# Performance work log

Hardware: AMD Instinct MI355X
Metric: run time of the kernel (lower is better)

Reference implementation:

```python
import jax, jax.numpy as jnp
import numpy as np

THRESHOLD = 1.0
BETA = 0.9  # initial mem is zeros, so mem = beta*0 + u = u


def spike(u):
    # forward of SurrogateGradient: (u > threshold).float()
    return (u > THRESHOLD).astype(u.dtype)


def rope_tables(seq_len, head_dim, base=10000.0):
    inv_freq = 1.0 / (base ** (jnp.arange(0, head_dim, 2, dtype=jnp.float32) / head_dim))
    t = jnp.arange(seq_len, dtype=jnp.float32)
    freqs = jnp.einsum('i,j->ij', t, inv_freq)          # [S, d/2]
    emb = jnp.concatenate([freqs, freqs], axis=-1)       # [S, d]
    return jnp.cos(emb), jnp.sin(emb)


def apply_rope(x, cos, sin):
    # x: [B, S, H, d]
    x1, x2 = jnp.split(x, 2, axis=-1)
    rot = jnp.concatenate([-x2, x1], axis=-1)
    return x * cos[None, :, None, :] + rot * sin[None, :, None, :]


def setup_inputs() -> dict:
    key = jax.random.key(0)
    ks = jax.random.split(key, 5)
    B, S, D = 1, 2048, 2048
    std = 1.0 / np.sqrt(D)
    return {
        'x':  jax.random.normal(ks[0], (B, S, D), jnp.float32),
        'Wq': jax.random.normal(ks[1], (D, D), jnp.float32) * std,
        'Wk': jax.random.normal(ks[2], (D, D), jnp.float32) * std,
        'Wv': jax.random.normal(ks[3], (D, D), jnp.float32) * std,
        'Wo': jax.random.normal(ks[4], (D, D), jnp.float32) * std,
    }


def reference(x, Wq, Wk, Wv, Wo):
    B, S, D = x.shape
    H, hd = 16, 128
    scale = hd ** -0.5

    q = (x @ Wq).reshape(B, S, H, hd)
    k = (x @ Wk).reshape(B, S, H, hd)
    v = (x @ Wv).reshape(B, S, H, hd)

    # LIF: mem starts at zero -> mem = q; spike = (mem > threshold)
    sq, sk, sv = spike(q), spike(k), spike(v)

    cos, sin = rope_tables(S, hd)
    rq = apply_rope(sq, cos, sin)
    rk = apply_rope(sk, cos, sin)

    scores = jnp.einsum('bqhd,bkhd->bhqk', rq, rk) * scale  # [B,H,S,S]
    causal = jnp.tril(jnp.ones((S, S), dtype=bool))
    scores = jnp.where(causal[None, None], scores, -jnp.inf)
    attn = jax.nn.softmax(scores, axis=-1)

    out = jnp.einsum('bhqk,bkhd->bqhd', attn, sv).reshape(B, S, H * hd)
    return out @ Wo
```

## Files before the change

kernel.cpp:

```cpp
#include <hip/hip_runtime.h>

typedef unsigned short u16;
typedef unsigned int u32;
typedef u16 u16x4 __attribute__((ext_vector_type(4)));
typedef u16 u16x8 __attribute__((ext_vector_type(8)));
typedef float f32x4 __attribute__((ext_vector_type(4)));
typedef __bf16 bf16x8 __attribute__((ext_vector_type(8)));
typedef _Float16 f16x4 __attribute__((ext_vector_type(4)));
typedef _Float16 f16x8 __attribute__((ext_vector_type(8)));

#define DD 2048
#define SCALE_ATTN 0.08838834764831845f
#define DELTA 0.005f

#define GL16(g, l)                                                              \
  __builtin_amdgcn_global_load_lds((const __attribute__((address_space(1))) u32*)(g), \
                                   (__attribute__((address_space(3))) u32*)(l), 16, 0, 0)

__device__ __forceinline__ u16 f2bf(float f) {
  u32 u = __float_as_uint(f);
  u32 r = (u + 0x7FFFu + ((u >> 16) & 1u)) >> 16;
  return (u16)r;
}
__device__ __forceinline__ float bf2f(u16 h) { return __uint_as_float(((u32)h) << 16); }


__global__ void k_rope_tables(float* __restrict__ cosT, float* __restrict__ sinT) {
  int i = blockIdx.x * 256 + threadIdx.x;
  int s = i >> 6, j = i & 63;
  float e = (float)(2 * j) / 128.0f;
  float inv = 1.0f / powf(10000.0f, e);
  float fr = (float)s * inv;
  cosT[i] = cosf(fr);
  sinT[i] = sinf(fr);
}

__global__ void k_cvt_x(const float* __restrict__ x, _Float16* __restrict__ xf) {
  int i = (blockIdx.x * 256 + threadIdx.x) * 4;
  float4 v = *(const float4*)&x[i];
  f16x4 o = {(_Float16)v.x, (_Float16)v.y, (_Float16)v.z, (_Float16)v.w};
  *(f16x4*)&xf[i] = o;
}

__global__ void k_transpose_w(const float* __restrict__ Wq, const float* __restrict__ Wk,
                              const float* __restrict__ Wv, _Float16* __restrict__ Wq16,
                              _Float16* __restrict__ Wk16, _Float16* __restrict__ Wv16,
                              float* __restrict__ Wq32, float* __restrict__ Wk32,
                              float* __restrict__ Wv32) {
  const float* W = blockIdx.y == 0 ? Wq : (blockIdx.y == 1 ? Wk : Wv);
  _Float16* WT16 = blockIdx.y == 0 ? Wq16 : (blockIdx.y == 1 ? Wk16 : Wv16);
  float* WT32 = blockIdx.y == 0 ? Wq32 : (blockIdx.y == 1 ? Wk32 : Wv32);
  __shared__ float tile[32][33];
  int bk = blockIdx.x & 63, bn = blockIdx.x >> 6;
  int c = threadIdx.x & 31, r0 = threadIdx.x >> 5;
#pragma unroll
  for (int i = 0; i < 4; ++i) {
    int r = r0 + i * 8;
    tile[r][c] = W[(size_t)(bk * 32 + r) * DD + bn * 32 + c];
  }
  __syncthreads();
#pragma unroll
  for (int i = 0; i < 4; ++i) {
    int r = r0 + i * 8;
    float v = tile[c][r];
    size_t o = (size_t)(bn * 32 + r) * DD + bk * 32 + c;
    WT16[o] = (_Float16)v;
    WT32[o] = v;
  }
}

__global__ void k_transpose_bo(const float* __restrict__ W, u16* __restrict__ WhT) {
  __shared__ float tile[32][33];
  int bk = blockIdx.x & 63, bn = blockIdx.x >> 6;
  int c = threadIdx.x & 31, r0 = threadIdx.x >> 5;
#pragma unroll
  for (int i = 0; i < 4; ++i) {
    int r = r0 + i * 8;
    tile[r][c] = W[(size_t)(bk * 32 + r) * DD + bn * 32 + c];
  }
  __syncthreads();
#pragma unroll
  for (int i = 0; i < 4; ++i) {
    int r = r0 + i * 8;
    WhT[(size_t)(bn * 32 + r) * DD + bk * 32 + c] = f2bf(tile[c][r]);
  }
}

__global__ void k_transpose_bf16(const u16* __restrict__ in, u16* __restrict__ out) {
  __shared__ u16 tile[32][33];
  int bk = blockIdx.x & 63, bn = blockIdx.x >> 6;
  int c = threadIdx.x & 31, r0 = threadIdx.x >> 5;
#pragma unroll
  for (int i = 0; i < 4; ++i) {
    int r = r0 + i * 8;
    tile[r][c] = in[(size_t)(bk * 32 + r) * DD + bn * 32 + c];
  }
  __syncthreads();
#pragma unroll
  for (int i = 0; i < 4; ++i) {
    int r = r0 + i * 8;
    out[(size_t)(bn * 32 + r) * DD + bk * 32 + c] = tile[c][r];
  }
}

__global__ void k_rope_apply(u16* sq, u16* sk, const float* __restrict__ cosT,
                             const float* __restrict__ sinT) {
  int i = blockIdx.x * 256 + threadIdx.x;
  int s = i >> 10;
  int rest = i & 1023;
  int h = rest >> 6, j = rest & 63;
  size_t base = (size_t)s * DD + h * 128 + j;
  float c = cosT[(s << 6) | j], sn = sinT[(s << 6) | j];
  float a = bf2f(sq[base]), b = bf2f(sq[base + 64]);
  sq[base] = f2bf(a * c - b * sn);
  sq[base + 64] = f2bf(b * c + a * sn);
  a = bf2f(sk[base]);
  b = bf2f(sk[base + 64]);
  sk[base] = f2bf(a * c - b * sn);
  sk[base + 64] = f2bf(b * c + a * sn);
}

__global__ __launch_bounds__(256) void k_gemm_qkv(
    const _Float16* __restrict__ xf, const _Float16* __restrict__ BqT,
    const _Float16* __restrict__ BkT, const _Float16* __restrict__ BvT, u16* __restrict__ Sq,
    u16* __restrict__ Sk, u16* __restrict__ Sv, unsigned char* __restrict__ flagT) {
  __shared__ u16 lA[2 * 4096];
  __shared__ u16 lB[2 * 4096];

  const _Float16* BT = blockIdx.y == 0 ? BqT : (blockIdx.y == 1 ? BkT : BvT);
  u16* Out = blockIdx.y == 0 ? Sq : (blockIdx.y == 1 ? Sk : Sv);
  unsigned char* flT = flagT + (size_t)blockIdx.y * 4194304;

  int bid = blockIdx.x;
  int swz = (bid & 7) * 32 + (bid >> 3);
  int m0 = (swz >> 4) * 128, n0 = (swz & 15) * 128;

  int tid = threadIdx.x;
  int lane = tid & 63;
  int w = tid >> 6;
  int wr = (w >> 1) * 64, wc = (w & 1) * 64;
  int l15 = lane & 15, g8 = (lane >> 4) * 8;

  int ar0 = tid >> 2, ac0 = (tid & 3) << 3;
  int ar1 = (tid + 256) >> 2, ac1 = (tid & 3) << 3;

  f32x4 zero = {0.f, 0.f, 0.f, 0.f};
  f32x4 acc[4][4];
#pragma unroll
  for (int i = 0; i < 4; ++i)
#pragma unroll
    for (int j = 0; j < 4; ++j) acc[i][j] = zero;

  u16* laBase0 = lA + w * 512;
  u16* laBase1 = lA + 2048 + w * 512;
  u16* lbBase0 = lB + w * 512;
  u16* lbBase1 = lB + 2048 + w * 512;

  auto stage = [&](int buf, int vs) {
    int k0 = vs << 5;
    int bo = buf * 4096;
    GL16(&xf[(size_t)(m0 + ar0) * DD + k0 + ac0], laBase0 + bo);
    GL16(&xf[(size_t)(m0 + ar1) * DD + k0 + ac1], laBase1 + bo);
    GL16(&BT[(size_t)(n0 + ar0) * DD + k0 + ac0], lbBase0 + bo);
    GL16(&BT[(size_t)(n0 + ar1) * DD + k0 + ac1], lbBase1 + bo);
  };

  stage(0, 0);
  __syncthreads();
  for (int vs = 0; vs < 64; ++vs) {
    int cur = vs & 1;
    if (vs + 1 < 64) stage(cur ^ 1, vs + 1);
    const u16* la = lA + cur * 4096;
    const u16* lb = lB + cur * 4096;
    f16x8 af[4], bfr[4];
#pragma unroll
    for (int i = 0; i < 4; ++i) af[i] = *(const f16x8*)&la[(wr + i * 16 + l15) * 32 + g8];
#pragma unroll
    for (int j = 0; j < 4; ++j) bfr[j] = *(const f16x8*)&lb[(wc + j * 16 + l15) * 32 + g8];
#pragma unroll
    for (int i = 0; i < 4; ++i)
#pragma unroll
      for (int j = 0; j < 4; ++j)
        acc[i][j] = __builtin_amdgcn_mfma_f32_16x16x32_f16(af[i], bfr[j], acc[i][j], 0, 0, 0);
    __syncthreads();
  }

  int g4 = (lane >> 4) * 4;
#pragma unroll
  for (int i = 0; i < 4; ++i) {
    int row0 = m0 + wr + i * 16 + g4;
#pragma unroll
    for (int j = 0; j < 4; ++j) {
      int col = n0 + wc + j * 16 + l15;
      u32 fw = 0;
#pragma unroll
      for (int r = 0; r < 4; ++r) {
        float u = acc[i][j][r];
        Out[(size_t)(row0 + r) * DD + col] = (u > 1.0f) ? (u16)0x3F80 : (u16)0;
        if (fabsf(u - 1.0f) < DELTA) fw |= (1u << (8 * r));
      }
      *(u32*)&flT[(size_t)col * 2048 + row0] = fw;
    }
  }
}

__global__ __launch_bounds__(256) void k_compact(const unsigned char* __restrict__ flagT,
                                                 u32* __restrict__ cnt, u32* __restrict__ wlist) {
  __shared__ u32 wsum[4];
  int tid = threadIdx.x;
  int lane = tid & 63;
  int w = tid >> 6;
  size_t blockBase = (size_t)blockIdx.x * 16384;
  const u32* fp = (const u32*)(flagT + blockBase);
  unsigned long long fm = 0;
#pragma unroll
  for (int it = 0; it < 4; ++it) {
    u32 m16 = 0;
#pragma unroll
    for (int wd = 0; wd < 4; ++wd) {
      u32 v = fp[it * 1024 + tid * 4 + wd];
      m16 |= (((v >> 0) & 1u) | ((v >> 7) & 2u) | ((v >> 14) & 4u) | ((v >> 21) & 8u)) << (wd * 4);
    }
    fm |= (unsigned long long)m16 << (it * 16);
  }
  u32 c = (u32)__popcll(fm);
  u32 pre = c;
#pragma unroll
  for (int d = 1; d < 64; d <<= 1) {
    u32 t = __shfl_up(pre, d, 64);
    if (lane >= d) pre += t;
  }
  if (lane == 63) wsum[w] = pre;
  __syncthreads();
  u32 wbase = 0;
#pragma unroll
  for (int i = 0; i < 4; ++i)
    if (i < w) wbase += wsum[i];
  if (tid == 0) {
    u32 tot = wsum[0] + wsum[1] + wsum[2] + wsum[3];
    cnt[blockIdx.x] = tot > 256u ? 256u : tot;
  }
  u32 pos = wbase + pre - c;
  u32 outbase = (u32)blockIdx.x * 256u;
  while (fm) {
    int p = __ffsll((long long)fm) - 1;
    fm &= fm - 1;
    u32 e = (u32)blockBase + (u32)(p >> 4) * 4096u + (u32)tid * 16u + (u32)(p & 15);
    if (pos < 256u) wlist[outbase + pos] = e;
    ++pos;
  }
}

__global__ __launch_bounds__(256) void k_fixup(
    const float* __restrict__ x, const float* __restrict__ WqT, const float* __restrict__ WkT,
    const float* __restrict__ WvT, const u32* __restrict__ cnt, const u32* __restrict__ wlist,
    u16* __restrict__ Sq, u16* __restrict__ Sk, u16* __restrict__ Sv) {
  u32 wid = (blockIdx.x * 256 + threadIdx.x) >> 6;
  int lane = threadIdx.x & 63;
  for (u32 s = wid; s < 768u * 256u; s += 8192u) {
    u32 b = s % 768u, k = s / 768u;
    if (k >= cnt[b]) continue;
    u32 e = wlist[b * 256u + k];
    int i = (int)(e & 2047u);
    int j = (int)((e >> 11) & 2047u);
    int mat = (int)(e >> 22);
    const float* WT = mat == 0 ? WqT : (mat == 1 ? WkT : WvT);
    const float* xr = x + (size_t)i * DD;
    const float* wrw = WT + (size_t)j * DD;
    float u = 0.f;
#pragma unroll
    for (int t = 0; t < 8; ++t) {
      float4 a = *(const float4*)&xr[t * 256 + lane * 4];
      float4 bv = *(const float4*)&wrw[t * 256 + lane * 4];
      u = fmaf(a.x, bv.x, u);
      u = fmaf(a.y, bv.y, u);
      u = fmaf(a.z, bv.z, u);
      u = fmaf(a.w, bv.w, u);
    }
#pragma unroll
    for (int sh = 32; sh; sh >>= 1) u += __shfl_xor(u, sh);
    if (lane == 0) {
      u16* Out2 = mat == 0 ? Sq : (mat == 1 ? Sk : Sv);
      Out2[(size_t)i * DD + j] = (u > 1.0f) ? (u16)0x3F80 : (u16)0;
    }
  }
}

__global__ __launch_bounds__(256) void k_gemm_out(const u16* __restrict__ A,
                                                  const u16* __restrict__ BT,
                                                  float* __restrict__ C) {
  __shared__ u16 lA[2 * 4096];
  __shared__ u16 lB[2 * 4096];
  int bid = blockIdx.x;
  int swz = (bid & 7) * 32 + (bid >> 3);
  int m0 = (swz >> 4) * 128, n0 = (swz & 15) * 128;
  int tid = threadIdx.x;
  int lane = tid & 63;
  int w = tid >> 6;
  int wr = (w >> 1) * 64, wc = (w & 1) * 64;
  int l15 = lane & 15, g8 = (lane >> 4) * 8;
  int ar0 = tid >> 2, ac0 = (tid & 3) << 3;
  int ar1 = (tid + 256) >> 2, ac1 = (tid & 3) << 3;
  f32x4 zero = {0.f, 0.f, 0.f, 0.f};
  f32x4 acc[4][4];
#pragma unroll
  for (int i = 0; i < 4; ++i)
#pragma unroll
    for (int j = 0; j < 4; ++j) acc[i][j] = zero;

  u16* laBase0 = lA + w * 512;
  u16* laBase1 = lA + 2048 + w * 512;
  u16* lbBase0 = lB + w * 512;
  u16* lbBase1 = lB + 2048 + w * 512;

  auto stage = [&](int buf, int vs) {
    int k0 = vs << 5;
    int bo = buf * 4096;
    GL16(&A[(size_t)(m0 + ar0) * DD + k0 + ac0], laBase0 + bo);
    GL16(&A[(size_t)(m0 + ar1) * DD + k0 + ac1], laBase1 + bo);
    GL16(&BT[(size_t)(n0 + ar0) * DD + k0 + ac0], lbBase0 + bo);
    GL16(&BT[(size_t)(n0 + ar1) * DD + k0 + ac1], lbBase1 + bo);
  };

  stage(0, 0);
  __syncthreads();
  for (int vs = 0; vs < 64; ++vs) {
    int cur = vs & 1;
    if (vs + 1 < 64) stage(cur ^ 1, vs + 1);
    const u16* la = lA + cur * 4096;
    const u16* lb = lB + cur * 4096;
    bf16x8 af[4], bfr[4];
#pragma unroll
    for (int i = 0; i < 4; ++i) af[i] = *(const bf16x8*)&la[(wr + i * 16 + l15) * 32 + g8];
#pragma unroll
    for (int j = 0; j < 4; ++j) bfr[j] = *(const bf16x8*)&lb[(wc + j * 16 + l15) * 32 + g8];
#pragma unroll
    for (int i = 0; i < 4; ++i)
#pragma unroll
      for (int j = 0; j < 4; ++j)
        acc[i][j] = __builtin_amdgcn_mfma_f32_16x16x32_bf16(af[i], bfr[j], acc[i][j], 0, 0, 0);
    __syncthreads();
  }

  int g4 = (lane >> 4) * 4;
#pragma unroll
  for (int i = 0; i < 4; ++i) {
    int row0 = m0 + wr + i * 16 + g4;
#pragma unroll
    for (int j = 0; j < 4; ++j) {
      int col = n0 + wc + j * 16 + l15;
#pragma unroll
      for (int r = 0; r < 4; ++r) C[(size_t)(row0 + r) * DD + col] = acc[i][j][r];
    }
  }
}

__global__ __launch_bounds__(256) void k_attn(const u16* __restrict__ rq,
                                              const u16* __restrict__ rk,
                                              const u16* __restrict__ svT,
                                              u16* __restrict__ outp) {
  __shared__ u16 lrk[64 * 136];
  __shared__ u16 lsv[128 * 72];
  __shared__ u16 lP[4 * 16 * 72];

  int bid = blockIdx.x;
  int h = bid & 15;
  int i0 = bid >> 4;
  int qb = 31 - i0;
  int q0 = qb * 64;

  int tid = threadIdx.x;
  int lane = tid & 63;
  int w = tid >> 6;
  int l15 = lane & 15;
  int g = lane >> 4;
  int qw = q0 + w * 16;
  int qpos = qw + l15;
  int pb = w * 1152 + l15 * 72;

  bf16x8 rqf[4];
#pragma unroll
  for (int ks = 0; ks < 4; ++ks)
    rqf[ks] = *(const bf16x8*)&rq[(size_t)qpos * DD + h * 128 + ks * 32 + g * 8];

  f32x4 zero = {0.f, 0.f, 0.f, 0.f};
  f32x4 acc[8];
#pragma unroll
  for (int dt = 0; dt < 8; ++dt) acc[dt] = zero;
  float mrun = -1e30f, lrun = 0.f;

  int nt = (q0 >> 6) + 1;
  for (int t = 0; t < nt; ++t) {
    int kv0 = t << 6;
    u16x8 sk_[4], sv_[4];
#pragma unroll
    for (int p = 0; p < 4; ++p) {
      int idx = tid + p * 256;
      int r = idx >> 4, c8 = (idx & 15) << 3;
      sk_[p] = *(const u16x8*)&rk[(size_t)(kv0 + r) * DD + h * 128 + c8];
      int r2 = idx >> 3, d8 = (idx & 7) << 3;
      sv_[p] = *(const u16x8*)&svT[(size_t)(h * 128 + r2) * DD + kv0 + d8];
    }
    __syncthreads();
#pragma unroll
    for (int p = 0; p < 4; ++p) {
      int idx = tid + p * 256;
      int r = idx >> 4, c8 = (idx & 15) << 3;
      *(u16x8*)&lrk[r * 136 + c8] = sk_[p];
      int r2 = idx >> 3, d8 = (idx & 7) << 3;
      *(u16x8*)&lsv[r2 * 72 + d8] = sv_[p];
    }
    __syncthreads();

    f32x4 sacc[4];
#pragma unroll
    for (int kt = 0; kt < 4; ++kt) sacc[kt] = zero;
#pragma unroll
    for (int kt = 0; kt < 4; ++kt)
#pragma unroll
      for (int ks = 0; ks < 4; ++ks) {
        bf16x8 a = *(const bf16x8*)&lrk[(kt * 16 + l15) * 136 + ks * 32 + g * 8];
        sacc[kt] = __builtin_amdgcn_mfma_f32_16x16x32_bf16(a, rqf[ks], sacc[kt], 0, 0, 0);
      }
    float p[4][4];
    float mx = -1e30f;
#pragma unroll
    for (int kt = 0; kt < 4; ++kt)
#pragma unroll
      for (int rr = 0; rr < 4; ++rr) {
        int kvpos = kv0 + kt * 16 + g * 4 + rr;
        float sc = sacc[kt][rr] * SCALE_ATTN;
        sc = (kvpos <= qpos) ? sc : -1e30f;
        p[kt][rr] = sc;
        mx = fmaxf(mx, sc);
      }
    mx = fmaxf(mx, __shfl_xor(mx, 16));
    mx = fmaxf(mx, __shfl_xor(mx, 32));
    float mnew = fmaxf(mrun, mx);
    float alpha = __expf(mrun - mnew);
    float rs = 0.f;
#pragma unroll
    for (int kt = 0; kt < 4; ++kt)
#pragma unroll
      for (int rr = 0; rr < 4; ++rr) {
        float e = __expf(p[kt][rr] - mnew);
        p[kt][rr] = e;
        rs += e;
      }
    rs += __shfl_xor(rs, 16);
    rs += __shfl_xor(rs, 32);
    lrun = lrun * alpha + rs;
    mrun = mnew;
    float al[4];
#pragma unroll
    for (int rr = 0; rr < 4; ++rr) al[rr] = __shfl(alpha, (lane & 48) | (g * 4 + rr), 64);
#pragma unroll
    for (int dt = 0; dt < 8; ++dt)
#pragma unroll
      for (int rr = 0; rr < 4; ++rr) acc[dt][rr] *= al[rr];
#pragma unroll
    for (int kt = 0; kt < 4; ++kt) {
      u16x4 pk = {f2bf(p[kt][0]), f2bf(p[kt][1]), f2bf(p[kt][2]), f2bf(p[kt][3])};
      *(u16x4*)&lP[pb + kt * 16 + g * 4] = pk;
    }
    bf16x8 pa0 = *(const bf16x8*)&lP[pb + g * 8];
    bf16x8 pa1 = *(const bf16x8*)&lP[pb + 32 + g * 8];
#pragma unroll
    for (int dt = 0; dt < 8; ++dt) {
      bf16x8 b0 = *(const bf16x8*)&lsv[(dt * 16 + l15) * 72 + g * 8];
      acc[dt] = __builtin_amdgcn_mfma_f32_16x16x32_bf16(pa0, b0, acc[dt], 0, 0, 0);
      bf16x8 b1 = *(const bf16x8*)&lsv[(dt * 16 + l15) * 72 + 32 + g * 8];
      acc[dt] = __builtin_amdgcn_mfma_f32_16x16x32_bf16(pa1, b1, acc[dt], 0, 0, 0);
    }
  }

  float linv[4];
#pragma unroll
  for (int rr = 0; rr < 4; ++rr)
    linv[rr] = 1.0f / __shfl(lrun, (lane & 48) | (g * 4 + rr), 64);
#pragma unroll
  for (int dt = 0; dt < 8; ++dt)
#pragma unroll
    for (int rr = 0; rr < 4; ++rr) {
      int row = qw + g * 4 + rr;
      outp[(size_t)row * DD + h * 128 + dt * 16 + l15] = f2bf(acc[dt][rr] * linv[rr]);
    }
}

extern "C" void kernel_launch(void* const* d_in, const int* in_sizes, int n_in, void* d_out,
                              int out_size, void* d_ws, size_t ws_size, hipStream_t stream) {
  (void)in_sizes;
  (void)n_in;
  (void)out_size;
  const float* x = (const float*)d_in[0];
  const float* Wq = (const float*)d_in[1];
  const float* Wk = (const float*)d_in[2];
  const float* Wv = (const float*)d_in[3];
  const float* Wo = (const float*)d_in[4];
  float* out = (float*)d_out;

  const size_t SZ = (size_t)DD * DD;
  size_t need = 35 * SZ + 2 * (size_t)2048 * 64 * 4;
  if (ws_size < need) return;

  char* p = (char*)d_ws;
  auto a2 = [&](void) {
    void* q = (void*)p;
    p += SZ * 2;
    return q;
  };
  _Float16* xf = (_Float16*)a2();
  _Float16* WqT16 = (_Float16*)a2();
  _Float16* WkT16 = (_Float16*)a2();
  _Float16* WvT16 = (_Float16*)a2();
  u16* BoT = (u16*)a2();
  u16* sq = (u16*)a2();
  u16* sk = (u16*)a2();
  u16* sv = (u16*)a2();
  u16* svT = (u16*)a2();
  u16* outp = (u16*)a2();
  float* WqT32 = (float*)p;
  p += SZ * 4;
  float* WkT32 = (float*)p;
  p += SZ * 4;
  float* WvT32 = (float*)p;
  p += SZ * 4;
  unsigned char* flagT = (unsigned char*)p;
  p += 3 * SZ;
  float* cosT = (float*)p;
  p += (size_t)2048 * 64 * 4;
  float* sinT = (float*)p;
  u32* cnt = (u32*)svT;
  u32* wlist = cnt + 1024;

  k_rope_tables<<<512, 256, 0, stream>>>(cosT, sinT);
  k_cvt_x<<<4096, 256, 0, stream>>>(x, xf);
  k_transpose_w<<<dim3(4096, 3, 1), 256, 0, stream>>>(Wq, Wk, Wv, WqT16, WkT16, WvT16, WqT32,
                                                      WkT32, WvT32);
  k_transpose_bo<<<4096, 256, 0, stream>>>(Wo, BoT);
  k_gemm_qkv<<<dim3(256, 3, 1), 256, 0, stream>>>(xf, WqT16, WkT16, WvT16, sq, sk, sv, flagT);
  k_compact<<<768, 256, 0, stream>>>(flagT, cnt, wlist);
  k_fixup<<<2048, 256, 0, stream>>>(x, WqT32, WkT32, WvT32, cnt, wlist, sq, sk, sv);
  k_rope_apply<<<8192, 256, 0, stream>>>(sq, sk, cosT, sinT);
  k_transpose_bf16<<<4096, 256, 0, stream>>>(sv, svT);
  k_attn<<<512, 256, 0, stream>>>(sq, sk, svT, outp);
  k_gemm_out<<<256, 256, 0, stream>>>(outp, BoT, out);
}
```

Baseline: 307.1 us.

## Merge small prep kernels and prefetch next KV tile in attention loop

Folds the RoPE table generation into the x-conversion kernel, merges the Wo transpose into the QKV weight transpose launch, and combines the RoPE apply and V transpose into one kernel. This cuts the launch count from eleven to eight. The attention loop now issues global loads for the next K/V tile right after the LDS store, so they overlap the current tile's MFMA and softmax work. The prefetch holds more registers live and could lower occupancy in the attention kernel.

```diff
diff --git a/kernel.cpp b/kernel.cpp
--- a/kernel.cpp
+++ b/kernel.cpp
@@ -25,31 +25,31 @@
 __device__ __forceinline__ float bf2f(u16 h) { return __uint_as_float(((u32)h) << 16); }
 
 
-__global__ void k_rope_tables(float* __restrict__ cosT, float* __restrict__ sinT) {
-  int i = blockIdx.x * 256 + threadIdx.x;
-  int s = i >> 6, j = i & 63;
-  float e = (float)(2 * j) / 128.0f;
-  float inv = 1.0f / powf(10000.0f, e);
-  float fr = (float)s * inv;
-  cosT[i] = cosf(fr);
-  sinT[i] = sinf(fr);
-}
-
-__global__ void k_cvt_x(const float* __restrict__ x, _Float16* __restrict__ xf) {
-  int i = (blockIdx.x * 256 + threadIdx.x) * 4;
+__global__ void k_cvt_x(const float* __restrict__ x, _Float16* __restrict__ xf,
+                        float* __restrict__ cosT, float* __restrict__ sinT) {
+  int gi = blockIdx.x * 256 + threadIdx.x;
+  int i = gi * 4;
   float4 v = *(const float4*)&x[i];
   f16x4 o = {(_Float16)v.x, (_Float16)v.y, (_Float16)v.z, (_Float16)v.w};
   *(f16x4*)&xf[i] = o;
+  if (gi < 131072) {
+    int s = gi >> 6, j = gi & 63;
+    float e = (float)(2 * j) / 128.0f;
+    float inv = 1.0f / powf(10000.0f, e);
+    float fr = (float)s * inv;
+    cosT[gi] = cosf(fr);
+    sinT[gi] = sinf(fr);
+  }
 }
 
 __global__ void k_transpose_w(const float* __restrict__ Wq, const float* __restrict__ Wk,
-                              const float* __restrict__ Wv, _Float16* __restrict__ Wq16,
-                              _Float16* __restrict__ Wk16, _Float16* __restrict__ Wv16,
-                              float* __restrict__ Wq32, float* __restrict__ Wk32,
-                              float* __restrict__ Wv32) {
-  const float* W = blockIdx.y == 0 ? Wq : (blockIdx.y == 1 ? Wk : Wv);
-  _Float16* WT16 = blockIdx.y == 0 ? Wq16 : (blockIdx.y == 1 ? Wk16 : Wv16);
-  float* WT32 = blockIdx.y == 0 ? Wq32 : (blockIdx.y == 1 ? Wk32 : Wv32);
+                              const float* __restrict__ Wv, const float* __restrict__ Wo,
+                              _Float16* __restrict__ Wq16, _Float16* __restrict__ Wk16,
+                              _Float16* __restrict__ Wv16, float* __restrict__ Wq32,
+                              float* __restrict__ Wk32, float* __restrict__ Wv32,
+                              u16* __restrict__ BoT) {
+  int y = blockIdx.y;
+  const float* W = y == 0 ? Wq : (y == 1 ? Wk : (y == 2 ? Wv : Wo));
   __shared__ float tile[32][33];
   int bk = blockIdx.x & 63, bn = blockIdx.x >> 6;
   int c = threadIdx.x & 31, r0 = threadIdx.x >> 5;
@@ -59,65 +59,61 @@
     tile[r][c] = W[(size_t)(bk * 32 + r) * DD + bn * 32 + c];
   }
   __syncthreads();
-#pragma unroll
-  for (int i = 0; i < 4; ++i) {
-    int r = r0 + i * 8;
-    float v = tile[c][r];
-    size_t o = (size_t)(bn * 32 + r) * DD + bk * 32 + c;
-    WT16[o] = (_Float16)v;
-    WT32[o] = v;
-  }
-}
-
-__global__ void k_transpose_bo(const float* __restrict__ W, u16* __restrict__ WhT) {
-  __shared__ float tile[32][33];
-  int bk = blockIdx.x & 63, bn = blockIdx.x >> 6;
-  int c = threadIdx.x & 31, r0 = threadIdx.x >> 5;
-#pragma unroll
-  for (int i = 0; i < 4; ++i) {
-    int r = r0 + i * 8;
-    tile[r][c] = W[(size_t)(bk * 32 + r) * DD + bn * 32 + c];
-  }
-  __syncthreads();
-#pragma unroll
-  for (int i = 0; i < 4; ++i) {
-    int r = r0 + i * 8;
-    WhT[(size_t)(bn * 32 + r) * DD + bk * 32 + c] = f2bf(tile[c][r]);
-  }
-}
-
-__global__ void k_transpose_bf16(const u16* __restrict__ in, u16* __restrict__ out) {
+  if (y < 3) {
+    _Float16* WT16 = y == 0 ? Wq16 : (y == 1 ? Wk16 : Wv16);
+    float* WT32 = y == 0 ? Wq32 : (y == 1 ? Wk32 : Wv32);
+#pragma unroll
+    for (int i = 0; i < 4; ++i) {
+      int r = r0 + i * 8;
+      float v = tile[c][r];
+      size_t o = (size_t)(bn * 32 + r) * DD + bk * 32 + c;
+      WT16[o] = (_Float16)v;
+      WT32[o] = v;
+    }
+  } else {
+#pragma unroll
+    for (int i = 0; i < 4; ++i) {
+      int r = r0 + i * 8;
+      BoT[(size_t)(bn * 32 + r) * DD + bk * 32 + c] = f2bf(tile[c][r]);
+    }
+  }
+}
+
+__global__ void k_post(u16* sq, u16* sk, const float* __restrict__ cosT,
+                       const float* __restrict__ sinT, const u16* __restrict__ sv,
+                       u16* __restrict__ svT) {
   __shared__ u16 tile[32][33];
-  int bk = blockIdx.x & 63, bn = blockIdx.x >> 6;
-  int c = threadIdx.x & 31, r0 = threadIdx.x >> 5;
-#pragma unroll
-  for (int i = 0; i < 4; ++i) {
-    int r = r0 + i * 8;
-    tile[r][c] = in[(size_t)(bk * 32 + r) * DD + bn * 32 + c];
-  }
-  __syncthreads();
-#pragma unroll
-  for (int i = 0; i < 4; ++i) {
-    int r = r0 + i * 8;
-    out[(size_t)(bn * 32 + r) * DD + bk * 32 + c] = tile[c][r];
-  }
-}
-
-__global__ void k_rope_apply(u16* sq, u16* sk, const float* __restrict__ cosT,
-                             const float* __restrict__ sinT) {
-  int i = blockIdx.x * 256 + threadIdx.x;
-  int s = i >> 10;
-  int rest = i & 1023;
-  int h = rest >> 6, j = rest & 63;
-  size_t base = (size_t)s * DD + h * 128 + j;
-  float c = cosT[(s << 6) | j], sn = sinT[(s << 6) | j];
-  float a = bf2f(sq[base]), b = bf2f(sq[base + 64]);
-  sq[base] = f2bf(a * c - b * sn);
-  sq[base + 64] = f2bf(b * c + a * sn);
-  a = bf2f(sk[base]);
-  b = bf2f(sk[base + 64]);
-  sk[base] = f2bf(a * c - b * sn);
-  sk[base + 64] = f2bf(b * c + a * sn);
+  int bid = blockIdx.x;
+  if (bid < 8192) {
+    int i = bid * 256 + threadIdx.x;
+    int s = i >> 10;
+    int rest = i & 1023;
+    int h = rest >> 6, j = rest & 63;
+    size_t base = (size_t)s * DD + h * 128 + j;
+    float c = cosT[(s << 6) | j], sn = sinT[(s << 6) | j];
+    float a = bf2f(sq[base]), b = bf2f(sq[base + 64]);
+    sq[base] = f2bf(a * c - b * sn);
+    sq[base + 64] = f2bf(b * c + a * sn);
+    a = bf2f(sk[base]);
+    b = bf2f(sk[base + 64]);
+    sk[base] = f2bf(a * c - b * sn);
+    sk[base + 64] = f2bf(b * c + a * sn);
+  } else {
+    int b = bid - 8192;
+    int bk = b & 63, bn = b >> 6;
+    int c = threadIdx.x & 31, r0 = threadIdx.x >> 5;
+#pragma unroll
+    for (int i = 0; i < 4; ++i) {
+      int r = r0 + i * 8;
+      tile[r][c] = sv[(size_t)(bk * 32 + r) * DD + bn * 32 + c];
+    }
+    __syncthreads();
+#pragma unroll
+    for (int i = 0; i < 4; ++i) {
+      int r = r0 + i * 8;
+      svT[(size_t)(bn * 32 + r) * DD + bk * 32 + c] = tile[c][r];
+    }
+  }
 }
 
 __global__ __launch_bounds__(256) void k_gemm_qkv(
@@ -389,10 +385,9 @@
   for (int dt = 0; dt < 8; ++dt) acc[dt] = zero;
   float mrun = -1e30f, lrun = 0.f;
 
-  int nt = (q0 >> 6) + 1;
-  for (int t = 0; t < nt; ++t) {
+  u16x8 sk_[4], sv_[4];
+  auto issue = [&](int t) {
     int kv0 = t << 6;
-    u16x8 sk_[4], sv_[4];
 #pragma unroll
     for (int p = 0; p < 4; ++p) {
       int idx = tid + p * 256;
@@ -401,6 +396,12 @@
       int r2 = idx >> 3, d8 = (idx & 7) << 3;
       sv_[p] = *(const u16x8*)&svT[(size_t)(h * 128 + r2) * DD + kv0 + d8];
     }
+  };
+
+  int nt = (q0 >> 6) + 1;
+  issue(0);
+  for (int t = 0; t < nt; ++t) {
+    int kv0 = t << 6;
     __syncthreads();
 #pragma unroll
     for (int p = 0; p < 4; ++p) {
@@ -411,6 +412,7 @@
       *(u16x8*)&lsv[r2 * 72 + d8] = sv_[p];
     }
     __syncthreads();
+    if (t + 1 < nt) issue(t + 1);
 
     f32x4 sacc[4];
 #pragma unroll
@@ -533,16 +535,13 @@
   u32* cnt = (u32*)svT;
   u32* wlist = cnt + 1024;
 
-  k_rope_tables<<<512, 256, 0, stream>>>(cosT, sinT);
-  k_cvt_x<<<4096, 256, 0, stream>>>(x, xf);
-  k_transpose_w<<<dim3(4096, 3, 1), 256, 0, stream>>>(Wq, Wk, Wv, WqT16, WkT16, WvT16, WqT32,
-                                                      WkT32, WvT32);
-  k_transpose_bo<<<4096, 256, 0, stream>>>(Wo, BoT);
+  k_cvt_x<<<4096, 256, 0, stream>>>(x, xf, cosT, sinT);
+  k_transpose_w<<<dim3(4096, 4, 1), 256, 0, stream>>>(Wq, Wk, Wv, Wo, WqT16, WkT16, WvT16,
+                                                      WqT32, WkT32, WvT32, BoT);
   k_gemm_qkv<<<dim3(256, 3, 1), 256, 0, stream>>>(xf, WqT16, WkT16, WvT16, sq, sk, sv, flagT);
   k_compact<<<768, 256, 0, stream>>>(flagT, cnt, wlist);
   k_fixup<<<2048, 256, 0, stream>>>(x, WqT32, WkT32, WvT32, cnt, wlist, sq, sk, sv);
-  k_rope_apply<<<8192, 256, 0, stream>>>(sq, sk, cosT, sinT);
-  k_transpose_bf16<<<4096, 256, 0, stream>>>(sv, svT);
+  k_post<<<12288, 256, 0, stream>>>(sq, sk, cosT, sinT, sv, svT);
   k_attn<<<512, 256, 0, stream>>>(sq, sk, svT, outp);
   k_gemm_out<<<256, 256, 0, stream>>>(outp, BoT, out);
 }
```

New measurement: 290.6 us. 1.06x faster.
